# Kernel tuning notes

Hardware: AMD Instinct MI355X
Metric: run time of the kernel (lower is better)

## Reference

```python
import jax, jax.numpy as jnp
import numpy as np

NEG = float(-2**32 + 1)
LN_EPS = 1e-5

def setup_inputs() -> dict:
    key = jax.random.key(0)
    ks = jax.random.split(key, 10)
    B, Sq, Sk, D = 8, 1024, 1024, 1024
    memory = jax.random.normal(ks[0], (B, Sk, D), jnp.float32)
    decoder_input = jax.random.normal(ks[1], (B, Sq, D), jnp.float32)
    query_mask = jax.random.uniform(ks[2], (B, Sq), jnp.float32)
    Wk = jax.random.normal(ks[3], (D, D), jnp.float32) * 0.02
    Wv = jax.random.normal(ks[4], (D, D), jnp.float32) * 0.02
    Wq = jax.random.normal(ks[5], (D, D), jnp.float32) * 0.02
    Wf = jax.random.normal(ks[6], (2 * D, D), jnp.float32) * 0.02
    bf = jnp.zeros((D,), jnp.float32)
    gamma = jnp.ones((D,), jnp.float32)
    beta = jnp.zeros((D,), jnp.float32)
    mask = jax.random.randint(ks[7], (B, Sq, Sk), 0, 2) == 1
    return dict(memory=memory, decoder_input=decoder_input, query_mask=query_mask,
                Wk=Wk, Wv=Wv, Wq=Wq, Wf=Wf, bf=bf, gamma=gamma, beta=beta, mask=mask)

def reference(memory, decoder_input, query_mask, Wk, Wv, Wq, Wf, bf, gamma, beta, mask):
    B, Sk, D = memory.shape
    Sq = decoder_input.shape[1]
    h = 8
    dh = D // h
    # projections (no bias), split heads -> [h, B, S, dh]
    K = (memory @ Wk).reshape(B, Sk, h, dh).transpose(2, 0, 1, 3)
    V = (memory @ Wv).reshape(B, Sk, h, dh).transpose(2, 0, 1, 3)
    Q = (decoder_input @ Wq).reshape(B, Sq, h, dh).transpose(2, 0, 1, 3)
    # scores [h, B, Sq, Sk]
    attn = jnp.einsum('hbqd,hbkd->hbqk', Q, K) / jnp.sqrt(jnp.float32(dh))
    attn = jnp.where(mask[None], NEG, attn)
    attn = jax.nn.softmax(attn, axis=-1)
    # non-standard post-softmax query-mask multiply
    attn = attn * query_mask[None, :, :, None]
    x = jnp.einsum('hbqk,hbkd->hbqd', attn, V)      # [h,B,Sq,dh]
    x = x.transpose(1, 2, 0, 3).reshape(B, Sq, D)    # concat heads
    x = jnp.concatenate([decoder_input, x], axis=-1)  # [B,Sq,2D]
    x = x @ Wf + bf
    x = x + decoder_input
    # LayerNorm
    mu = jnp.mean(x, axis=-1, keepdims=True)
    var = jnp.var(x, axis=-1, keepdims=True)
    x = (x - mu) * jax.lax.rsqrt(var + LN_EPS) * gamma + beta
    attns = attn.reshape(h * B, Sq, Sk)  # match torch layout [h*B,Sq,Sk]
    return x, attns
```

## Files before the change

### kernel.cpp

```cpp
#include <hip/hip_runtime.h>
#include <hip/hip_bf16.h>
#include <stdint.h>

typedef __attribute__((ext_vector_type(4))) float  floatx4;
typedef __attribute__((ext_vector_type(8))) short  shortx8;

__device__ __forceinline__ unsigned short f2bf(float f) {
    unsigned int u = __builtin_bit_cast(unsigned int, f);
    u += 0x7FFFu + ((u >> 16) & 1u);
    return (unsigned short)(u >> 16);
}
__device__ __forceinline__ float bf2f(unsigned short h) {
    unsigned int u = (unsigned int)h << 16;
    return __builtin_bit_cast(float, u);
}

__device__ __forceinline__ uint4 pack8(float4 a, float4 b) {
    uint4 r;
    r.x = (unsigned)f2bf(a.x) | ((unsigned)f2bf(a.y) << 16);
    r.y = (unsigned)f2bf(a.z) | ((unsigned)f2bf(a.w) << 16);
    r.z = (unsigned)f2bf(b.x) | ((unsigned)f2bf(b.y) << 16);
    r.w = (unsigned)f2bf(b.z) | ((unsigned)f2bf(b.w) << 16);
    return r;
}

__device__ __forceinline__ void gload16(const ushort* g, ushort* l) {
    __builtin_amdgcn_global_load_lds(
        (const __attribute__((address_space(1))) unsigned int*)g,
        (__attribute__((address_space(3))) unsigned int*)l, 16, 0, 0);
}

__global__ __launch_bounds__(256) void cast_both(const float* __restrict__ mem,
                                                 const float* __restrict__ dec,
                                                 ushort* __restrict__ mem_bf,
                                                 ushort* __restrict__ concat) {
    if (blockIdx.x < 4096) {
        long long i = ((long long)blockIdx.x * 256 + threadIdx.x) * 8;
        const float4* p = (const float4*)(mem + i);
        *(uint4*)(mem_bf + i) = pack8(p[0], p[1]);
    } else {
        long long i = ((long long)(blockIdx.x - 4096) * 256 + threadIdx.x) * 8;
        long long r = i >> 10, c = i & 1023;
        const float4* p = (const float4*)(dec + i);
        *(uint4*)(concat + r * 2048 + c) = pack8(p[0], p[1]);
    }
}

__global__ __launch_bounds__(256) void pack_mask(const int* __restrict__ mask,
                                                 unsigned long long* __restrict__ mb) {
    int gw = (blockIdx.x * 256 + threadIdx.x) >> 6;
    int l = threadIdx.x & 63;
    #pragma unroll
    for (int i = 0; i < 16; ++i) {
        size_t widx = (size_t)gw * 16 + i;
        unsigned long long m = __ballot(mask[widx * 64 + l] != 0);
        if (l == 0) mb[widx] = m;
    }
}

__global__ __launch_bounds__(256) void wtrans(const float* __restrict__ W,
                                              ushort* __restrict__ WT, int K, int N) {
    __shared__ float t[32][33];
    int tx = threadIdx.x, ty = threadIdx.y;
    int bx = blockIdx.x * 32;
    int by = blockIdx.y * 32;
    #pragma unroll
    for (int i = 0; i < 4; i++)
        t[ty + 8 * i][tx] = W[(size_t)(by + ty + 8 * i) * N + bx + tx];
    __syncthreads();
    #pragma unroll
    for (int i = 0; i < 4; i++)
        WT[(size_t)(bx + ty + 8 * i) * K + by + tx] = f2bf(t[tx][ty + 8 * i]);
}

__global__ __launch_bounds__(256) void wtrans3(const float* __restrict__ W0,
                                               const float* __restrict__ W1,
                                               const float* __restrict__ W2,
                                               ushort* __restrict__ T0,
                                               ushort* __restrict__ T1,
                                               ushort* __restrict__ T2) {
    __shared__ float t[32][33];
    const float* W = blockIdx.z == 0 ? W0 : (blockIdx.z == 1 ? W1 : W2);
    ushort* WT     = blockIdx.z == 0 ? T0 : (blockIdx.z == 1 ? T1 : T2);
    int tx = threadIdx.x, ty = threadIdx.y;
    int bx = blockIdx.x * 32;
    int by = blockIdx.y * 32;
    #pragma unroll
    for (int i = 0; i < 4; i++)
        t[ty + 8 * i][tx] = W[(size_t)(by + ty + 8 * i) * 1024 + bx + tx];
    __syncthreads();
    #pragma unroll
    for (int i = 0; i < 4; i++)
        WT[(size_t)(bx + ty + 8 * i) * 1024 + by + tx] = f2bf(t[tx][ty + 8 * i]);
}

__global__ __launch_bounds__(256) void vtrans(const ushort* __restrict__ V,
                                              ushort* __restrict__ VT) {
    __shared__ ushort t[32][33];
    int tx = threadIdx.x, ty = threadIdx.y;
    int bk = blockIdx.x * 32;
    int bd = blockIdx.y * 32;
    int z = blockIdx.z;
    int b = z >> 3, h = z & 7;
    #pragma unroll
    for (int i = 0; i < 4; i++)
        t[ty + 8 * i][tx] = V[((size_t)(b * 1024 + bk + ty + 8 * i)) * 1024 + h * 128 + bd + tx];
    __syncthreads();
    #pragma unroll
    for (int i = 0; i < 4; i++)
        VT[((size_t)((h * 8 + b) * 128 + bd + ty + 8 * i)) * 1024 + bk + tx] = t[tx][ty + 8 * i];
}

template <typename TC>
__device__ __forceinline__ void gemm_core(ushort* As, ushort* Bs,
                                          const ushort* __restrict__ A,
                                          const ushort* __restrict__ Bt, TC* __restrict__ C,
                                          int kbeg, int kend, int lda, int ldb, int ldc,
                                          int bm, int bn) {
    int tid = threadIdx.x;
    int l = tid & 63, wid = tid >> 6;
    int l16 = l & 15, quad = l >> 4;
    int wm = (wid & 1) * 64, wn = (wid >> 1) * 64;
    int srow = tid >> 3;
    int scol = (tid & 7) * 8;

    floatx4 acc[4][4];
    #pragma unroll
    for (int i = 0; i < 4; i++)
        #pragma unroll
        for (int j = 0; j < 4; j++)
            acc[i][j] = {0.0f, 0.0f, 0.0f, 0.0f};

    for (int kt = kbeg; kt < kend; kt += 64) {
        #pragma unroll
        for (int it = 0; it < 4; it++) {
            int row = it * 32 + srow;
            gload16(A + (size_t)(bm + row) * lda + kt + scol, &As[row * 64 + scol]);
            gload16(Bt + (size_t)(bn + row) * ldb + kt + scol, &Bs[row * 64 + scol]);
        }
        __syncthreads();
        #pragma unroll
        for (int kk = 0; kk < 64; kk += 32) {
            shortx8 af[4], bfr[4];
            #pragma unroll
            for (int i = 0; i < 4; i++)
                af[i] = *(const shortx8*)&As[(wm + i * 16 + l16) * 64 + kk + quad * 8];
            #pragma unroll
            for (int j = 0; j < 4; j++)
                bfr[j] = *(const shortx8*)&Bs[(wn + j * 16 + l16) * 64 + kk + quad * 8];
            #pragma unroll
            for (int i = 0; i < 4; i++)
                #pragma unroll
                for (int j = 0; j < 4; j++)
                    acc[i][j] = __builtin_amdgcn_mfma_f32_16x16x32_bf16(af[i], bfr[j], acc[i][j], 0, 0, 0);
        }
        __syncthreads();
    }

    #pragma unroll
    for (int i = 0; i < 4; i++) {
        #pragma unroll
        for (int j = 0; j < 4; j++) {
            int row0 = bm + wm + i * 16 + quad * 4;
            int col = bn + wn + j * 16 + l16;
            #pragma unroll
            for (int r = 0; r < 4; r++) {
                float v = acc[i][j][r];
                size_t idx = (size_t)(row0 + r) * ldc + col;
                if constexpr (__is_same(TC, float)) C[idx] = v;
                else C[idx] = f2bf(v);
            }
        }
    }
}

__global__ __launch_bounds__(256) void gemm_proj3(
    const ushort* __restrict__ mem_bf, const ushort* __restrict__ concat,
    const ushort* __restrict__ WkT, const ushort* __restrict__ WvT,
    const ushort* __restrict__ WqT,
    ushort* __restrict__ Kp, ushort* __restrict__ Vp, ushort* __restrict__ Qp) {
    __shared__ ushort As[128 * 64];
    __shared__ ushort Bs[128 * 64];
    const ushort* A; const ushort* Bt; ushort* C; int lda;
    if (blockIdx.z == 0)      { A = mem_bf; Bt = WkT; C = Kp; lda = 1024; }
    else if (blockIdx.z == 1) { A = mem_bf; Bt = WvT; C = Vp; lda = 1024; }
    else                      { A = concat; Bt = WqT; C = Qp; lda = 2048; }
    gemm_core<ushort>(As, Bs, A, Bt, C, 0, 1024, lda, 1024, 1024,
                      blockIdx.y * 128, blockIdx.x * 128);
}

__global__ __launch_bounds__(256) void gemm_ffn(
    const ushort* __restrict__ concat, const ushort* __restrict__ WfT,
    float* __restrict__ ffn0, float* __restrict__ ffn1) {
    __shared__ ushort As[128 * 64];
    __shared__ ushort Bs[128 * 64];
    int z = blockIdx.z;
    gemm_core<float>(As, Bs, concat, WfT, z ? ffn1 : ffn0,
                     z * 1024, z * 1024 + 1024, 2048, 2048, 1024,
                     blockIdx.y * 128, blockIdx.x * 128);
}

__global__ __launch_bounds__(256, 4) void fused_attn(
    const ushort* __restrict__ Qp, const ushort* __restrict__ Kp,
    const ushort* __restrict__ VT, const unsigned long long* __restrict__ mb,
    const float* __restrict__ qmask, float* __restrict__ attns,
    ushort* __restrict__ concat) {
    __shared__ ushort Qs[16 * 136];
    __shared__ ushort Ss[16 * 1032];
    __shared__ unsigned Ms[16][34];
    __shared__ float rowpart[16][5];
    __shared__ float scale_s[16];

    const int b = blockIdx.z, h = blockIdx.y, q0 = blockIdx.x * 16;
    const int tid = threadIdx.x;
    const int w = tid >> 6, l = tid & 63;
    const int l16 = l & 15, quad = l >> 4;
    const float sc = 0.08838834764831845f;

    {
        int row = tid >> 4, col = (tid & 15) * 8;
        *(uint4*)&Qs[row * 136 + col] =
            *(const uint4*)(Qp + (size_t)(b * 1024 + q0 + row) * 1024 + h * 128 + col);
        int pr = tid & 15;
        uint2 mv = ((const uint2*)mb)[(size_t)(b * 1024 + q0 + row) * 16 + pr];
        Ms[row][pr * 2] = mv.x;
        Ms[row][pr * 2 + 1] = mv.y;
    }
    __syncthreads();

    shortx8 af[4];
    #pragma unroll
    for (int kk = 0; kk < 4; kk++)
        af[kk] = *(const shortx8*)&Qs[l16 * 136 + kk * 32 + quad * 8];

    const ushort* Kb = Kp + (size_t)(b * 1024 + w * 16 + l16) * 1024 + h * 128 + quad * 8;
    shortx8 kf0 = *(const shortx8*)(Kb + 0);
    shortx8 kf1 = *(const shortx8*)(Kb + 32);
    shortx8 kf2 = *(const shortx8*)(Kb + 64);
    shortx8 kf3 = *(const shortx8*)(Kb + 96);
    float ssum[4] = {0.0f, 0.0f, 0.0f, 0.0f};
    const int bp64 = w * 16 + l16;
    const int wsel = bp64 >> 5, bitp = bp64 & 31;
    for (int c = 0; c < 16; ++c) {
        int cn = c < 15 ? c + 1 : c;
        const ushort* Kn = Kb + (size_t)cn * 65536;
        shortx8 kn0 = *(const shortx8*)(Kn + 0);
        shortx8 kn1 = *(const shortx8*)(Kn + 32);
        shortx8 kn2 = *(const shortx8*)(Kn + 64);
        shortx8 kn3 = *(const shortx8*)(Kn + 96);
        floatx4 acc = {0.0f, 0.0f, 0.0f, 0.0f};
        __builtin_amdgcn_s_setprio(1);
        acc = __builtin_amdgcn_mfma_f32_16x16x32_bf16(af[0], kf0, acc, 0, 0, 0);
        acc = __builtin_amdgcn_mfma_f32_16x16x32_bf16(af[1], kf1, acc, 0, 0, 0);
        acc = __builtin_amdgcn_mfma_f32_16x16x32_bf16(af[2], kf2, acc, 0, 0, 0);
        acc = __builtin_amdgcn_mfma_f32_16x16x32_bf16(af[3], kf3, acc, 0, 0, 0);
        __builtin_amdgcn_s_setprio(0);
        int k0 = c * 64 + w * 16;
        #pragma unroll
        for (int r = 0; r < 4; ++r) {
            int q = quad * 4 + r;
            unsigned wv = Ms[q][c * 2 + wsel];
            float v = ((wv >> bitp) & 1u) ? 0.0f : __expf(acc[r] * sc);
            ssum[r] += v;
            Ss[q * 1032 + k0 + l16] = f2bf(v);
        }
        kf0 = kn0; kf1 = kn1; kf2 = kn2; kf3 = kn3;
    }

    #pragma unroll
    for (int r = 0; r < 4; ++r) {
        float s = ssum[r];
        #pragma unroll
        for (int off = 1; off < 16; off <<= 1) s += __shfl_xor(s, off, 16);
        ssum[r] = s;
    }
    if (l16 == 0) {
        #pragma unroll
        for (int r = 0; r < 4; ++r) rowpart[quad * 4 + r][w] = ssum[r];
    }
    __syncthreads();
    if (tid < 16) {
        float s = rowpart[tid][0] + rowpart[tid][1] + rowpart[tid][2] + rowpart[tid][3];
        scale_s[tid] = qmask[b * 1024 + q0 + tid] / s;
    }
    __syncthreads();

    {
        int row = tid >> 4;
        float scl = scale_s[row];
        float* arow = attns + ((size_t)((h * 8 + b) * 1024 + q0 + row)) * 1024;
        int c0 = (tid & 15) * 4;
        #pragma unroll
        for (int j = 0; j < 16; ++j) {
            int c = c0 + j * 64;
            ushort4 v = *(const ushort4*)&Ss[row * 1032 + c];
            floatx4 o;
            o.x = bf2f(v.x) * scl;
            o.y = bf2f(v.y) * scl;
            o.z = bf2f(v.z) * scl;
            o.w = bf2f(v.w) * scl;
            __builtin_nontemporal_store(o, (floatx4*)(arow + c));
        }
    }

    const size_t vrow0 = (size_t)((h * 8 + b) * 128 + w * 32);
    const ushort* Vb0 = VT + (vrow0 + l16) * 1024 + quad * 8;
    const ushort* Vb1 = VT + (vrow0 + 16 + l16) * 1024 + quad * 8;
    shortx8 v00 = *(const shortx8*)(Vb0);
    shortx8 v01 = *(const shortx8*)(Vb1);
    shortx8 v10 = *(const shortx8*)(Vb0 + 32);
    shortx8 v11 = *(const shortx8*)(Vb1 + 32);
    floatx4 o0 = {0.0f, 0.0f, 0.0f, 0.0f}, o1 = {0.0f, 0.0f, 0.0f, 0.0f};
    for (int c = 0; c < 16; ++c) {
        int cn = c < 15 ? c + 1 : c;
        shortx8 n00 = *(const shortx8*)(Vb0 + cn * 64);
        shortx8 n01 = *(const shortx8*)(Vb1 + cn * 64);
        shortx8 n10 = *(const shortx8*)(Vb0 + cn * 64 + 32);
        shortx8 n11 = *(const shortx8*)(Vb1 + cn * 64 + 32);
        shortx8 pa0 = *(const shortx8*)&Ss[l16 * 1032 + c * 64 + quad * 8];
        shortx8 pa1 = *(const shortx8*)&Ss[l16 * 1032 + c * 64 + 32 + quad * 8];
        __builtin_amdgcn_s_setprio(1);
        o0 = __builtin_amdgcn_mfma_f32_16x16x32_bf16(pa0, v00, o0, 0, 0, 0);
        o1 = __builtin_amdgcn_mfma_f32_16x16x32_bf16(pa0, v01, o1, 0, 0, 0);
        o0 = __builtin_amdgcn_mfma_f32_16x16x32_bf16(pa1, v10, o0, 0, 0, 0);
        o1 = __builtin_amdgcn_mfma_f32_16x16x32_bf16(pa1, v11, o1, 0, 0, 0);
        __builtin_amdgcn_s_setprio(0);
        v00 = n00; v01 = n01; v10 = n10; v11 = n11;
    }
    #pragma unroll
    for (int r = 0; r < 4; ++r) {
        int q = quad * 4 + r;
        float scl = scale_s[q];
        int d = w * 32 + l16;
        size_t base = (size_t)(b * 1024 + q0 + q) * 2048 + 1024 + h * 128;
        concat[base + d]      = f2bf(o0[r] * scl);
        concat[base + d + 16] = f2bf(o1[r] * scl);
    }
}

__global__ __launch_bounds__(256) void ln_out(const float* __restrict__ ffn0,
                                              const float* __restrict__ ffn1,
                                              const float* __restrict__ dec,
                                              const float* __restrict__ bfv,
                                              const float* __restrict__ gamma,
                                              const float* __restrict__ beta,
                                              float* __restrict__ out) {
    __shared__ float sb[8];
    int row = blockIdx.x, tid = threadIdx.x;
    int c = tid * 4;
    size_t base = (size_t)row * 1024 + c;
    float4 x = *(const float4*)(ffn0 + base);
    float4 y = *(const float4*)(ffn1 + base);
    float4 d = *(const float4*)(dec + base);
    float4 bb = *(const float4*)(bfv + c);
    x.x += y.x + d.x + bb.x; x.y += y.y + d.y + bb.y;
    x.z += y.z + d.z + bb.z; x.w += y.w + d.w + bb.w;

    float s = x.x + x.y + x.z + x.w;
    float s2 = x.x * x.x + x.y * x.y + x.z * x.z + x.w * x.w;
    #pragma unroll
    for (int o = 32; o; o >>= 1) {
        s += __shfl_down(s, o, 64);
        s2 += __shfl_down(s2, o, 64);
    }
    if ((tid & 63) == 0) { sb[tid >> 6] = s; sb[4 + (tid >> 6)] = s2; }
    __syncthreads();
    s = sb[0] + sb[1] + sb[2] + sb[3];
    s2 = sb[4] + sb[5] + sb[6] + sb[7];
    float mu = s * (1.0f / 1024.0f);
    float var = s2 * (1.0f / 1024.0f) - mu * mu;
    float rs = rsqrtf(var + 1e-5f);

    float4 g = *(const float4*)(gamma + c);
    float4 be = *(const float4*)(beta + c);
    float4 o4;
    o4.x = (x.x - mu) * rs * g.x + be.x;
    o4.y = (x.y - mu) * rs * g.y + be.y;
    o4.z = (x.z - mu) * rs * g.z + be.z;
    o4.w = (x.w - mu) * rs * g.w + be.w;
    *(float4*)(out + base) = o4;
}

extern "C" void kernel_launch(void* const* d_in, const int* in_sizes, int n_in,
                              void* d_out, int out_size, void* d_ws, size_t ws_size,
                              hipStream_t stream) {
    const float* memory  = (const float*)d_in[0];
    const float* decoder = (const float*)d_in[1];
    const float* qmask   = (const float*)d_in[2];
    const float* Wk      = (const float*)d_in[3];
    const float* Wv      = (const float*)d_in[4];
    const float* Wq      = (const float*)d_in[5];
    const float* Wf      = (const float*)d_in[6];
    const float* bfv     = (const float*)d_in[7];
    const float* gamma   = (const float*)d_in[8];
    const float* beta    = (const float*)d_in[9];
    const int*   mask    = (const int*)d_in[10];

    float* xout  = (float*)d_out;
    float* attns = xout + 8388608LL;

    char* w = (char*)d_ws;
    ushort* mem_bf = (ushort*)(w + 0);
    ushort* Kp     = (ushort*)(w + (16LL << 20));
    ushort* Qp     = (ushort*)(w + (32LL << 20));
    ushort* Vp     = (ushort*)(w + (48LL << 20));
    ushort* VT     = (ushort*)(w + (64LL << 20));
    ushort* concat = (ushort*)(w + (80LL << 20));
    ushort* WkT    = (ushort*)(w + (112LL << 20));
    ushort* WvT    = (ushort*)(w + (114LL << 20));
    ushort* WqT    = (ushort*)(w + (116LL << 20));
    ushort* WfT    = (ushort*)(w + (118LL << 20));
    unsigned long long* mbits = (unsigned long long*)(w + (48LL << 20));
    float* ffn0 = (float*)(w + 0);
    float* ffn1 = (float*)(w + (32LL << 20));

    cast_both<<<8192, 256, 0, stream>>>(memory, decoder, mem_bf, concat);
    wtrans3<<<dim3(32, 32, 3), dim3(32, 8), 0, stream>>>(Wk, Wv, Wq, WkT, WvT, WqT);
    wtrans<<<dim3(32, 64), dim3(32, 8), 0, stream>>>(Wf, WfT, 2048, 1024);
    gemm_proj3<<<dim3(8, 64, 3), 256, 0, stream>>>(mem_bf, concat, WkT, WvT, WqT, Kp, Vp, Qp);
    vtrans<<<dim3(32, 4, 64), dim3(32, 8), 0, stream>>>(Vp, VT);
    pack_mask<<<2048, 256, 0, stream>>>(mask, mbits);
    fused_attn<<<dim3(64, 8, 8), 256, 0, stream>>>(Qp, Kp, VT, mbits, qmask, attns, concat);
    gemm_ffn<<<dim3(8, 64, 2), 256, 0, stream>>>(concat, WfT, ffn0, ffn1);
    ln_out<<<8192, 256, 0, stream>>>(ffn0, ffn1, decoder, bfv, gamma, beta, xout);
}
```

Baseline: 752.4 us.

## Merge prep kernels, remap blocks per XCD, deepen K/V prefetch in attention

```diff
diff --git a/kernel.cpp b/kernel.cpp
--- a/kernel.cpp
+++ b/kernel.cpp
@@ -30,68 +30,59 @@
         (__attribute__((address_space(3))) unsigned int*)l, 16, 0, 0);
 }
 
-__global__ __launch_bounds__(256) void cast_both(const float* __restrict__ mem,
+__global__ __launch_bounds__(256) void cast_pack(const float* __restrict__ mem,
                                                  const float* __restrict__ dec,
+                                                 const int* __restrict__ mask,
                                                  ushort* __restrict__ mem_bf,
-                                                 ushort* __restrict__ concat) {
-    if (blockIdx.x < 4096) {
-        long long i = ((long long)blockIdx.x * 256 + threadIdx.x) * 8;
+                                                 ushort* __restrict__ concat,
+                                                 unsigned long long* __restrict__ mb) {
+    int bx = blockIdx.x;
+    if (bx < 4096) {
+        long long i = ((long long)bx * 256 + threadIdx.x) * 8;
         const float4* p = (const float4*)(mem + i);
         *(uint4*)(mem_bf + i) = pack8(p[0], p[1]);
-    } else {
-        long long i = ((long long)(blockIdx.x - 4096) * 256 + threadIdx.x) * 8;
+    } else if (bx < 8192) {
+        long long i = ((long long)(bx - 4096) * 256 + threadIdx.x) * 8;
         long long r = i >> 10, c = i & 1023;
         const float4* p = (const float4*)(dec + i);
         *(uint4*)(concat + r * 2048 + c) = pack8(p[0], p[1]);
-    }
-}
-
-__global__ __launch_bounds__(256) void pack_mask(const int* __restrict__ mask,
-                                                 unsigned long long* __restrict__ mb) {
-    int gw = (blockIdx.x * 256 + threadIdx.x) >> 6;
-    int l = threadIdx.x & 63;
-    #pragma unroll
-    for (int i = 0; i < 16; ++i) {
-        size_t widx = (size_t)gw * 16 + i;
-        unsigned long long m = __ballot(mask[widx * 64 + l] != 0);
-        if (l == 0) mb[widx] = m;
-    }
-}
-
-__global__ __launch_bounds__(256) void wtrans(const float* __restrict__ W,
-                                              ushort* __restrict__ WT, int K, int N) {
+    } else {
+        int gw = ((bx - 8192) * 256 + threadIdx.x) >> 6;
+        int l = threadIdx.x & 63;
+        #pragma unroll
+        for (int i = 0; i < 16; ++i) {
+            size_t widx = (size_t)gw * 16 + i;
+            unsigned long long m = __ballot(mask[widx * 64 + l] != 0);
+            if (l == 0) mb[widx] = m;
+        }
+    }
+}
+
+__global__ __launch_bounds__(256) void wtrans_all(const float* __restrict__ W0,
+                                                  const float* __restrict__ W1,
+                                                  const float* __restrict__ W2,
+                                                  const float* __restrict__ W3,
+                                                  ushort* __restrict__ T0,
+                                                  ushort* __restrict__ T1,
+                                                  ushort* __restrict__ T2,
+                                                  ushort* __restrict__ T3) {
     __shared__ float t[32][33];
+    int z = blockIdx.z;
+    const float* W; ushort* WT; int K, byb;
+    if (z == 0)      { W = W0; WT = T0; K = 1024; byb = blockIdx.y; }
+    else if (z == 1) { W = W1; WT = T1; K = 1024; byb = blockIdx.y; }
+    else if (z == 2) { W = W2; WT = T2; K = 1024; byb = blockIdx.y; }
+    else             { W = W3; WT = T3; K = 2048; byb = blockIdx.y + (z - 3) * 32; }
     int tx = threadIdx.x, ty = threadIdx.y;
     int bx = blockIdx.x * 32;
-    int by = blockIdx.y * 32;
+    int by = byb * 32;
     #pragma unroll
     for (int i = 0; i < 4; i++)
-        t[ty + 8 * i][tx] = W[(size_t)(by + ty + 8 * i) * N + bx + tx];
+        t[ty + 8 * i][tx] = W[(size_t)(by + ty + 8 * i) * 1024 + bx + tx];
     __syncthreads();
     #pragma unroll
     for (int i = 0; i < 4; i++)
         WT[(size_t)(bx + ty + 8 * i) * K + by + tx] = f2bf(t[tx][ty + 8 * i]);
-}
-
-__global__ __launch_bounds__(256) void wtrans3(const float* __restrict__ W0,
-                                               const float* __restrict__ W1,
-                                               const float* __restrict__ W2,
-                                               ushort* __restrict__ T0,
-                                               ushort* __restrict__ T1,
-                                               ushort* __restrict__ T2) {
-    __shared__ float t[32][33];
-    const float* W = blockIdx.z == 0 ? W0 : (blockIdx.z == 1 ? W1 : W2);
-    ushort* WT     = blockIdx.z == 0 ? T0 : (blockIdx.z == 1 ? T1 : T2);
-    int tx = threadIdx.x, ty = threadIdx.y;
-    int bx = blockIdx.x * 32;
-    int by = blockIdx.y * 32;
-    #pragma unroll
-    for (int i = 0; i < 4; i++)
-        t[ty + 8 * i][tx] = W[(size_t)(by + ty + 8 * i) * 1024 + bx + tx];
-    __syncthreads();
-    #pragma unroll
-    for (int i = 0; i < 4; i++)
-        WT[(size_t)(bx + ty + 8 * i) * 1024 + by + tx] = f2bf(t[tx][ty + 8 * i]);
 }
 
 __global__ __launch_bounds__(256) void vtrans(const ushort* __restrict__ V,
@@ -181,12 +172,16 @@
     ushort* __restrict__ Kp, ushort* __restrict__ Vp, ushort* __restrict__ Qp) {
     __shared__ ushort As[128 * 64];
     __shared__ ushort Bs[128 * 64];
+    int bid = blockIdx.x;
+    int z = bid >> 9;
+    int r = bid & 511;
+    int xcd = r & 7, i = r >> 3;
+    int m = xcd * 8 + (i & 7), n = i >> 3;
     const ushort* A; const ushort* Bt; ushort* C; int lda;
-    if (blockIdx.z == 0)      { A = mem_bf; Bt = WkT; C = Kp; lda = 1024; }
-    else if (blockIdx.z == 1) { A = mem_bf; Bt = WvT; C = Vp; lda = 1024; }
-    else                      { A = concat; Bt = WqT; C = Qp; lda = 2048; }
-    gemm_core<ushort>(As, Bs, A, Bt, C, 0, 1024, lda, 1024, 1024,
-                      blockIdx.y * 128, blockIdx.x * 128);
+    if (z == 0)      { A = mem_bf; Bt = WkT; C = Kp; lda = 1024; }
+    else if (z == 1) { A = mem_bf; Bt = WvT; C = Vp; lda = 1024; }
+    else             { A = concat; Bt = WqT; C = Qp; lda = 2048; }
+    gemm_core<ushort>(As, Bs, A, Bt, C, 0, 1024, lda, 1024, 1024, m * 128, n * 128);
 }
 
 __global__ __launch_bounds__(256) void gemm_ffn(
@@ -194,10 +189,13 @@
     float* __restrict__ ffn0, float* __restrict__ ffn1) {
     __shared__ ushort As[128 * 64];
     __shared__ ushort Bs[128 * 64];
-    int z = blockIdx.z;
+    int bid = blockIdx.x;
+    int z = bid >> 9;
+    int r = bid & 511;
+    int xcd = r & 7, i = r >> 3;
+    int m = xcd * 8 + (i & 7), n = i >> 3;
     gemm_core<float>(As, Bs, concat, WfT, z ? ffn1 : ffn0,
-                     z * 1024, z * 1024 + 1024, 2048, 2048, 1024,
-                     blockIdx.y * 128, blockIdx.x * 128);
+                     z * 1024, z * 1024 + 1024, 2048, 2048, 1024, m * 128, n * 128);
 }
 
 __global__ __launch_bounds__(256, 4) void fused_attn(
@@ -211,7 +209,11 @@
     __shared__ float rowpart[16][5];
     __shared__ float scale_s[16];
 
-    const int b = blockIdx.z, h = blockIdx.y, q0 = blockIdx.x * 16;
+    int bid = blockIdx.x;
+    const int h = bid & 7;
+    int t = bid >> 3;
+    const int b = t >> 6;
+    const int q0 = (t & 63) * 16;
     const int tid = threadIdx.x;
     const int w = tid >> 6, l = tid & 63;
     const int l16 = l & 15, quad = l >> 4;
@@ -234,38 +236,58 @@
         af[kk] = *(const shortx8*)&Qs[l16 * 136 + kk * 32 + quad * 8];
 
     const ushort* Kb = Kp + (size_t)(b * 1024 + w * 16 + l16) * 1024 + h * 128 + quad * 8;
-    shortx8 kf0 = *(const shortx8*)(Kb + 0);
-    shortx8 kf1 = *(const shortx8*)(Kb + 32);
-    shortx8 kf2 = *(const shortx8*)(Kb + 64);
-    shortx8 kf3 = *(const shortx8*)(Kb + 96);
+#define KLD(c, o) (*(const shortx8*)(Kb + (size_t)(c) * 65536 + (o)))
+    shortx8 ka0 = KLD(0, 0), ka1 = KLD(0, 32), ka2 = KLD(0, 64), ka3 = KLD(0, 96);
+    shortx8 kb0 = KLD(1, 0), kb1 = KLD(1, 32), kb2 = KLD(1, 64), kb3 = KLD(1, 96);
     float ssum[4] = {0.0f, 0.0f, 0.0f, 0.0f};
     const int bp64 = w * 16 + l16;
     const int wsel = bp64 >> 5, bitp = bp64 & 31;
-    for (int c = 0; c < 16; ++c) {
-        int cn = c < 15 ? c + 1 : c;
-        const ushort* Kn = Kb + (size_t)cn * 65536;
-        shortx8 kn0 = *(const shortx8*)(Kn + 0);
-        shortx8 kn1 = *(const shortx8*)(Kn + 32);
-        shortx8 kn2 = *(const shortx8*)(Kn + 64);
-        shortx8 kn3 = *(const shortx8*)(Kn + 96);
+    #pragma unroll 1
+    for (int cc = 0; cc < 16; cc += 2) {
+        int c2 = cc + 2 < 16 ? cc + 2 : 14;
+        int c3 = cc + 3 < 16 ? cc + 3 : 15;
+        shortx8 n0 = KLD(c2, 0), n1 = KLD(c2, 32), n2 = KLD(c2, 64), n3 = KLD(c2, 96);
         floatx4 acc = {0.0f, 0.0f, 0.0f, 0.0f};
         __builtin_amdgcn_s_setprio(1);
-        acc = __builtin_amdgcn_mfma_f32_16x16x32_bf16(af[0], kf0, acc, 0, 0, 0);
-        acc = __builtin_amdgcn_mfma_f32_16x16x32_bf16(af[1], kf1, acc, 0, 0, 0);
-        acc = __builtin_amdgcn_mfma_f32_16x16x32_bf16(af[2], kf2, acc, 0, 0, 0);
-        acc = __builtin_amdgcn_mfma_f32_16x16x32_bf16(af[3], kf3, acc, 0, 0, 0);
+        acc = __builtin_amdgcn_mfma_f32_16x16x32_bf16(af[0], ka0, acc, 0, 0, 0);
+        acc = __builtin_amdgcn_mfma_f32_16x16x32_bf16(af[1], ka1, acc, 0, 0, 0);
+        acc = __builtin_amdgcn_mfma_f32_16x16x32_bf16(af[2], ka2, acc, 0, 0, 0);
+        acc = __builtin_amdgcn_mfma_f32_16x16x32_bf16(af[3], ka3, acc, 0, 0, 0);
         __builtin_amdgcn_s_setprio(0);
-        int k0 = c * 64 + w * 16;
-        #pragma unroll
-        for (int r = 0; r < 4; ++r) {
-            int q = quad * 4 + r;
-            unsigned wv = Ms[q][c * 2 + wsel];
-            float v = ((wv >> bitp) & 1u) ? 0.0f : __expf(acc[r] * sc);
-            ssum[r] += v;
-            Ss[q * 1032 + k0 + l16] = f2bf(v);
-        }
-        kf0 = kn0; kf1 = kn1; kf2 = kn2; kf3 = kn3;
-    }
+        {
+            int k0 = cc * 64 + w * 16;
+            #pragma unroll
+            for (int r = 0; r < 4; ++r) {
+                int q = quad * 4 + r;
+                unsigned wv = Ms[q][cc * 2 + wsel];
+                float v = ((wv >> bitp) & 1u) ? 0.0f : __expf(acc[r] * sc);
+                ssum[r] += v;
+                Ss[q * 1032 + k0 + l16] = f2bf(v);
+            }
+        }
+        shortx8 m0 = KLD(c3, 0), m1 = KLD(c3, 32), m2 = KLD(c3, 64), m3 = KLD(c3, 96);
+        floatx4 acc2 = {0.0f, 0.0f, 0.0f, 0.0f};
+        __builtin_amdgcn_s_setprio(1);
+        acc2 = __builtin_amdgcn_mfma_f32_16x16x32_bf16(af[0], kb0, acc2, 0, 0, 0);
+        acc2 = __builtin_amdgcn_mfma_f32_16x16x32_bf16(af[1], kb1, acc2, 0, 0, 0);
+        acc2 = __builtin_amdgcn_mfma_f32_16x16x32_bf16(af[2], kb2, acc2, 0, 0, 0);
+        acc2 = __builtin_amdgcn_mfma_f32_16x16x32_bf16(af[3], kb3, acc2, 0, 0, 0);
+        __builtin_amdgcn_s_setprio(0);
+        {
+            int k0 = (cc + 1) * 64 + w * 16;
+            #pragma unroll
+            for (int r = 0; r < 4; ++r) {
+                int q = quad * 4 + r;
+                unsigned wv = Ms[q][(cc + 1) * 2 + wsel];
+                float v = ((wv >> bitp) & 1u) ? 0.0f : __expf(acc2[r] * sc);
+                ssum[r] += v;
+                Ss[q * 1032 + k0 + l16] = f2bf(v);
+            }
+        }
+        ka0 = n0; ka1 = n1; ka2 = n2; ka3 = n3;
+        kb0 = m0; kb1 = m1; kb2 = m2; kb3 = m3;
+    }
+#undef KLD
 
     #pragma unroll
     for (int r = 0; r < 4; ++r) {
@@ -284,6 +306,15 @@
         scale_s[tid] = qmask[b * 1024 + q0 + tid] / s;
     }
     __syncthreads();
+
+    const size_t vrow0 = (size_t)((h * 8 + b) * 128 + w * 32);
+    const ushort* Vb0 = VT + (vrow0 + l16) * 1024 + quad * 8;
+    const ushort* Vb1 = VT + (vrow0 + 16 + l16) * 1024 + quad * 8;
+#define VLD(p, c, o) (*(const shortx8*)((p) + (c) * 64 + (o)))
+    shortx8 va0 = VLD(Vb0, 0, 0), va1 = VLD(Vb1, 0, 0);
+    shortx8 va2 = VLD(Vb0, 0, 32), va3 = VLD(Vb1, 0, 32);
+    shortx8 vb0 = VLD(Vb0, 1, 0), vb1 = VLD(Vb1, 1, 0);
+    shortx8 vb2 = VLD(Vb0, 1, 32), vb3 = VLD(Vb1, 1, 32);
 
     {
         int row = tid >> 4;
@@ -303,30 +334,35 @@
         }
     }
 
-    const size_t vrow0 = (size_t)((h * 8 + b) * 128 + w * 32);
-    const ushort* Vb0 = VT + (vrow0 + l16) * 1024 + quad * 8;
-    const ushort* Vb1 = VT + (vrow0 + 16 + l16) * 1024 + quad * 8;
-    shortx8 v00 = *(const shortx8*)(Vb0);
-    shortx8 v01 = *(const shortx8*)(Vb1);
-    shortx8 v10 = *(const shortx8*)(Vb0 + 32);
-    shortx8 v11 = *(const shortx8*)(Vb1 + 32);
     floatx4 o0 = {0.0f, 0.0f, 0.0f, 0.0f}, o1 = {0.0f, 0.0f, 0.0f, 0.0f};
-    for (int c = 0; c < 16; ++c) {
-        int cn = c < 15 ? c + 1 : c;
-        shortx8 n00 = *(const shortx8*)(Vb0 + cn * 64);
-        shortx8 n01 = *(const shortx8*)(Vb1 + cn * 64);
-        shortx8 n10 = *(const shortx8*)(Vb0 + cn * 64 + 32);
-        shortx8 n11 = *(const shortx8*)(Vb1 + cn * 64 + 32);
-        shortx8 pa0 = *(const shortx8*)&Ss[l16 * 1032 + c * 64 + quad * 8];
-        shortx8 pa1 = *(const shortx8*)&Ss[l16 * 1032 + c * 64 + 32 + quad * 8];
+    #pragma unroll 1
+    for (int cc = 0; cc < 16; cc += 2) {
+        int c2 = cc + 2 < 16 ? cc + 2 : 14;
+        int c3 = cc + 3 < 16 ? cc + 3 : 15;
+        shortx8 n0 = VLD(Vb0, c2, 0), n1 = VLD(Vb1, c2, 0);
+        shortx8 n2 = VLD(Vb0, c2, 32), n3 = VLD(Vb1, c2, 32);
+        shortx8 pa0 = *(const shortx8*)&Ss[l16 * 1032 + cc * 64 + quad * 8];
+        shortx8 pa1 = *(const shortx8*)&Ss[l16 * 1032 + cc * 64 + 32 + quad * 8];
         __builtin_amdgcn_s_setprio(1);
-        o0 = __builtin_amdgcn_mfma_f32_16x16x32_bf16(pa0, v00, o0, 0, 0, 0);
-        o1 = __builtin_amdgcn_mfma_f32_16x16x32_bf16(pa0, v01, o1, 0, 0, 0);
-        o0 = __builtin_amdgcn_mfma_f32_16x16x32_bf16(pa1, v10, o0, 0, 0, 0);
-        o1 = __builtin_amdgcn_mfma_f32_16x16x32_bf16(pa1, v11, o1, 0, 0, 0);
+        o0 = __builtin_amdgcn_mfma_f32_16x16x32_bf16(pa0, va0, o0, 0, 0, 0);
+        o1 = __builtin_amdgcn_mfma_f32_16x16x32_bf16(pa0, va1, o1, 0, 0, 0);
+        o0 = __builtin_amdgcn_mfma_f32_16x16x32_bf16(pa1, va2, o0, 0, 0, 0);
+        o1 = __builtin_amdgcn_mfma_f32_16x16x32_bf16(pa1, va3, o1, 0, 0, 0);
         __builtin_amdgcn_s_setprio(0);
-        v00 = n00; v01 = n01; v10 = n10; v11 = n11;
-    }
+        shortx8 m0 = VLD(Vb0, c3, 0), m1 = VLD(Vb1, c3, 0);
+        shortx8 m2 = VLD(Vb0, c3, 32), m3 = VLD(Vb1, c3, 32);
+        shortx8 pb0 = *(const shortx8*)&Ss[l16 * 1032 + (cc + 1) * 64 + quad * 8];
+        shortx8 pb1 = *(const shortx8*)&Ss[l16 * 1032 + (cc + 1) * 64 + 32 + quad * 8];
+        __builtin_amdgcn_s_setprio(1);
+        o0 = __builtin_amdgcn_mfma_f32_16x16x32_bf16(pb0, vb0, o0, 0, 0, 0);
+        o1 = __builtin_amdgcn_mfma_f32_16x16x32_bf16(pb0, vb1, o1, 0, 0, 0);
+        o0 = __builtin_amdgcn_mfma_f32_16x16x32_bf16(pb1, vb2, o0, 0, 0, 0);
+        o1 = __builtin_amdgcn_mfma_f32_16x16x32_bf16(pb1, vb3, o1, 0, 0, 0);
+        __builtin_amdgcn_s_setprio(0);
+        va0 = n0; va1 = n1; va2 = n2; va3 = n3;
+        vb0 = m0; vb1 = m1; vb2 = m2; vb3 = m3;
+    }
+#undef VLD
     #pragma unroll
     for (int r = 0; r < 4; ++r) {
         int q = quad * 4 + r;
@@ -410,17 +446,15 @@
     ushort* WvT    = (ushort*)(w + (114LL << 20));
     ushort* WqT    = (ushort*)(w + (116LL << 20));
     ushort* WfT    = (ushort*)(w + (118LL << 20));
-    unsigned long long* mbits = (unsigned long long*)(w + (48LL << 20));
+    unsigned long long* mbits = (unsigned long long*)(w + (122LL << 20));
     float* ffn0 = (float*)(w + 0);
     float* ffn1 = (float*)(w + (32LL << 20));
 
-    cast_both<<<8192, 256, 0, stream>>>(memory, decoder, mem_bf, concat);
-    wtrans3<<<dim3(32, 32, 3), dim3(32, 8), 0, stream>>>(Wk, Wv, Wq, WkT, WvT, WqT);
-    wtrans<<<dim3(32, 64), dim3(32, 8), 0, stream>>>(Wf, WfT, 2048, 1024);
-    gemm_proj3<<<dim3(8, 64, 3), 256, 0, stream>>>(mem_bf, concat, WkT, WvT, WqT, Kp, Vp, Qp);
+    cast_pack<<<10240, 256, 0, stream>>>(memory, decoder, mask, mem_bf, concat, mbits);
+    wtrans_all<<<dim3(32, 32, 5), dim3(32, 8), 0, stream>>>(Wk, Wv, Wq, Wf, WkT, WvT, WqT, WfT);
+    gemm_proj3<<<1536, 256, 0, stream>>>(mem_bf, concat, WkT, WvT, WqT, Kp, Vp, Qp);
     vtrans<<<dim3(32, 4, 64), dim3(32, 8), 0, stream>>>(Vp, VT);
-    pack_mask<<<2048, 256, 0, stream>>>(mask, mbits);
-    fused_attn<<<dim3(64, 8, 8), 256, 0, stream>>>(Qp, Kp, VT, mbits, qmask, attns, concat);
-    gemm_ffn<<<dim3(8, 64, 2), 256, 0, stream>>>(concat, WfT, ffn0, ffn1);
+    fused_attn<<<4096, 256, 0, stream>>>(Qp, Kp, VT, mbits, qmask, attns, concat);
+    gemm_ffn<<<1024, 256, 0, stream>>>(concat, WfT, ffn0, ffn1);
     ln_out<<<8192, 256, 0, stream>>>(ffn0, ffn1, decoder, bfv, gamma, beta, xout);
 }
```

Measured after the change: 770.7 us. 1.02x slower.
